# Performance work log

Measured on AMD Instinct MI355X. Metric: run time of the kernel, lower is better.

Reference implementation:

```python
import jax, jax.numpy as jnp
import numpy as np

B, T, C = 2, 4096, 1024
H = 16
D = C // H  # head_dim = 64


def setup_inputs() -> dict:
    key = jax.random.key(0)
    k1, k2, k3 = jax.random.split(key, 3)
    x = jax.random.normal(k1, (B, T, C), dtype=jnp.float32)
    W_qkv = jax.random.normal(k2, (3 * C, C), dtype=jnp.float32) * (1.0 / np.sqrt(C))
    W_out = jax.random.normal(k3, (C, C), dtype=jnp.float32) * (1.0 / np.sqrt(C))
    return {"x": x, "W_qkv": W_qkv, "W_out": W_out}


def reference(x, W_qkv, W_out):
    b, t, c = x.shape
    # qkv projection: torch Linear y = x @ W.T  -> (B,T,3C)
    qkv = jnp.einsum('btc,fc->btf', x, W_qkv)
    qkv = qkv.reshape(b, t, 3, H, D)
    q, k, v = qkv[:, :, 0], qkv[:, :, 1], qkv[:, :, 2]  # (B,T,H,D)
    q = q.transpose(0, 2, 1, 3)  # (B,H,T,D)
    k = k.transpose(0, 2, 1, 3)
    v = v.transpose(0, 2, 1, 3)
    scale = 1.0 / np.sqrt(D).astype(np.float32)
    att = jnp.einsum('bhqd,bhkd->bhqk', q, k) * scale  # (B,H,T,T)
    causal = jnp.tril(jnp.ones((t, t), dtype=bool))
    att = jnp.where(causal[None, None], att, jnp.float32(-jnp.inf))
    att = jax.nn.softmax(att, axis=-1)
    # dropout p=0.0 -> identity
    out = jnp.einsum('bhqk,bhkd->bhqd', att, v)  # (B,H,T,D)
    out = out.transpose(0, 2, 1, 3).reshape(b, t, c)
    return jnp.einsum('btc,oc->bto', out, W_out)
```

## Files before the change

kernel.cpp:

```cpp
#include <hip/hip_runtime.h>

constexpr int Bn = 2;
constexpr int Tn = 4096;
constexpr int Cn = 1024;
constexpr int Hn = 16;
constexpr int Dn = 64;

typedef __bf16 bf16x8 __attribute__((ext_vector_type(8)));
typedef float f32x4 __attribute__((ext_vector_type(4)));
typedef unsigned short u16x8 __attribute__((ext_vector_type(8)));

__device__ __forceinline__ unsigned short f2bf(float f) {
  unsigned int u = __float_as_uint(f);
  u += 0x7FFF + ((u >> 16) & 1);
  return (unsigned short)(u >> 16);
}

__device__ __forceinline__ unsigned short f2bf_hw(float f) {
  return __builtin_bit_cast(unsigned short, (__bf16)f);
}

__device__ __forceinline__ bf16x8 ld_bf8(const unsigned short* p) {
  return __builtin_bit_cast(bf16x8, *(const u16x8*)p);
}

__global__ void cvt_kernel(const float* __restrict__ in, unsigned short* __restrict__ out, int n4) {
  int i = blockIdx.x * blockDim.x + threadIdx.x;
  if (i >= n4) return;
  float4 v = ((const float4*)in)[i];
  ushort4 o;
  o.x = f2bf(v.x); o.y = f2bf(v.y); o.z = f2bf(v.z); o.w = f2bf(v.w);
  ((ushort4*)out)[i] = o;
}

template<int OUT_BF16>
__global__ __launch_bounds__(256) void gemm_bt(const unsigned short* __restrict__ A,
                                               const unsigned short* __restrict__ Bm,
                                               void* __restrict__ Cout,
                                               int M, int N, int K) {
  __shared__ __align__(16) unsigned short As[128][64];
  __shared__ __align__(16) unsigned short Bs[128][64];
  const int tid  = threadIdx.x;
  const int wave = tid >> 6;
  const int lane = tid & 63;
  const int wr   = (wave >> 1) * 64;
  const int wc   = (wave & 1) * 64;
  const int lrow = lane & 15;
  const int lk8  = (lane >> 4) << 3;

  const int nbx  = gridDim.x;
  const int nwg  = nbx * gridDim.y;
  const int orig = blockIdx.y * nbx + blockIdx.x;
  const int cid  = (orig & 7) * (nwg >> 3) + (orig >> 3);
  const int row0 = (cid / nbx) * 128;
  const int col0 = (cid % nbx) * 128;

  f32x4 acc[4][4];
  #pragma unroll
  for (int i = 0; i < 4; ++i)
    #pragma unroll
    for (int j = 0; j < 4; ++j)
      acc[i][j] = (f32x4){0.f, 0.f, 0.f, 0.f};

  for (int k0 = 0; k0 < K; k0 += 64) {
    const unsigned short* Ag = A  + (size_t)row0 * K + k0;
    const unsigned short* Bg = Bm + (size_t)col0 * K + k0;
    #pragma unroll
    for (int i = 0; i < 4; ++i) {
      int flat = (i * 256 + tid) * 8;
      int r = flat >> 6, c = flat & 63;
      __builtin_amdgcn_global_load_lds((const __attribute__((address_space(1))) void*)(Ag + (size_t)r * K + c),
                                       (__attribute__((address_space(3))) void*)(&As[r][c]), 16, 0, 0);
    }
    #pragma unroll
    for (int i = 0; i < 4; ++i) {
      int flat = (i * 256 + tid) * 8;
      int r = flat >> 6, c = flat & 63;
      __builtin_amdgcn_global_load_lds((const __attribute__((address_space(1))) void*)(Bg + (size_t)r * K + c),
                                       (__attribute__((address_space(3))) void*)(&Bs[r][c]), 16, 0, 0);
    }
    __syncthreads();

    #pragma unroll
    for (int ks = 0; ks < 2; ++ks) {
      bf16x8 af[4], bfr[4];
      #pragma unroll
      for (int i = 0; i < 4; ++i) af[i]  = ld_bf8(&As[wr + i * 16 + lrow][ks * 32 + lk8]);
      #pragma unroll
      for (int j = 0; j < 4; ++j) bfr[j] = ld_bf8(&Bs[wc + j * 16 + lrow][ks * 32 + lk8]);
      #pragma unroll
      for (int i = 0; i < 4; ++i)
        #pragma unroll
        for (int j = 0; j < 4; ++j)
          acc[i][j] = __builtin_amdgcn_mfma_f32_16x16x32_bf16(af[i], bfr[j], acc[i][j], 0, 0, 0);
    }
    __syncthreads();
  }

  const int rg = (lane >> 4) * 4;
  const int cl = lane & 15;
  #pragma unroll
  for (int i = 0; i < 4; ++i)
    #pragma unroll
    for (int j = 0; j < 4; ++j)
      #pragma unroll
      for (int rr = 0; rr < 4; ++rr) {
        int gm = row0 + wr + i * 16 + rg + rr;
        int gn = col0 + wc + j * 16 + cl;
        float v = acc[i][j][rr];
        if (OUT_BF16) ((unsigned short*)Cout)[(size_t)gm * N + gn] = f2bf(v);
        else          ((float*)Cout)[(size_t)gm * N + gn] = v;
      }
}

__global__ __launch_bounds__(256) void vtrans_kernel(const unsigned short* __restrict__ qkv,
                                                     unsigned short* __restrict__ vT) {
  __shared__ __align__(16) unsigned short L[64 * 64];
  const int tid = threadIdx.x;
  const int t0  = blockIdx.x * 64;
  const int bh  = blockIdx.y;
  const int b   = bh >> 4;
  const int h   = bh & 15;
  const unsigned short* src = qkv + (size_t)b * Tn * (3 * Cn) + 2 * Cn + h * Dn;

  #pragma unroll
  for (int i = 0; i < 2; ++i) {
    int flat = i * 256 + tid;
    int t = flat >> 3, c = flat & 7;
    int cs = c ^ ((t >> 3) & 7);
    __builtin_amdgcn_global_load_lds(
        (const __attribute__((address_space(1))) void*)(src + (size_t)(t0 + t) * (3 * Cn) + cs * 8),
        (__attribute__((address_space(3))) void*)(&L[flat * 8]), 16, 0, 0);
  }
  __syncthreads();

  #pragma unroll
  for (int i = 0; i < 2; ++i) {
    int flat = i * 256 + tid;
    int d = flat >> 3, tc = flat & 7;
    u16x8 o;
    #pragma unroll
    for (int j = 0; j < 8; ++j) {
      int t = tc * 8 + j;
      o[j] = L[t * 64 + (((d >> 3) ^ ((t >> 3) & 7)) << 3) + (d & 7)];
    }
    *(u16x8*)(vT + ((size_t)bh * 64 + d) * Tn + t0 + tc * 8) = o;
  }
}

__global__ __launch_bounds__(256) void attn_kernel(const unsigned short* __restrict__ qkv,
                                                   const unsigned short* __restrict__ vT,
                                                   unsigned short* __restrict__ outb) {
  __shared__ __align__(16) unsigned short Ks[2][4096];
  __shared__ __align__(16) unsigned short Vs[2][4096];
  __shared__ __align__(16) unsigned short Ps[4][1024];

  const int tid  = threadIdx.x;
  const int wave = tid >> 6;
  const int lane = tid & 63;
  const int cl   = lane & 15;
  const int g    = lane >> 4;
  const int lk8  = g << 3;
  const int rg   = g * 4;

  const int orig = blockIdx.y * gridDim.x + blockIdx.x;
  const int cid  = (orig & 7) * 256 + (orig >> 3);
  const int qt   = (63 - (cid & 63)) * 64;
  const int bh   = cid >> 6;
  const int b    = bh >> 4;
  const int h    = bh & 15;

  const unsigned short* qb  = qkv + (size_t)b * Tn * (3 * Cn) + h * Dn;
  const unsigned short* kb  = qb + Cn;
  const unsigned short* vtb = vT + (size_t)bh * Dn * Tn;

  bf16x8 qf[2];
  {
    const unsigned short* qr = qb + (size_t)(qt + wave * 16 + cl) * (3 * Cn) + lk8;
    qf[0] = ld_bf8(qr);
    qf[1] = ld_bf8(qr + 32);
    #pragma unroll
    for (int j = 0; j < 8; ++j) {
      qf[0][j] = qf[0][j] * (__bf16)0.125f;
      qf[1][j] = qf[1][j] * (__bf16)0.125f;
    }
  }

  f32x4 oacc[4];
  #pragma unroll
  for (int n = 0; n < 4; ++n) oacc[n] = (f32x4){0.f, 0.f, 0.f, 0.f};
  float mrun[4] = {-1e30f, -1e30f, -1e30f, -1e30f};
  float lrun[4] = {0.f, 0.f, 0.f, 0.f};

  #pragma unroll
  for (int i = 0; i < 2; ++i) {
    const int flat = i * 256 + tid;
    const int r    = flat >> 3;
    const int cg   = flat & 7;
    const int sw   = cg ^ (r & 7);
    __builtin_amdgcn_global_load_lds(
        (const __attribute__((address_space(1))) void*)(kb + (size_t)r * (3 * Cn) + sw * 8),
        (__attribute__((address_space(3))) void*)(&Ks[0][flat * 8]), 16, 0, 0);
    __builtin_amdgcn_global_load_lds(
        (const __attribute__((address_space(1))) void*)(vtb + (size_t)r * Tn + sw * 8),
        (__attribute__((address_space(3))) void*)(&Vs[0][flat * 8]), 16, 0, 0);
  }
  __syncthreads();

  const int nkv = qt / 64 + 1;
  for (int kt = 0; kt < nkv; ++kt) {
    const int kv0 = kt * 64;
    const int cur = kt & 1;
    const int nb  = cur ^ 1;
    const bool pre = (kt + 1 < nkv);

    if (pre) {
      const int kv1 = kv0 + 64;
      #pragma unroll
      for (int i = 0; i < 2; ++i) {
        const int flat = i * 256 + tid;
        const int r    = flat >> 3;
        const int cg   = flat & 7;
        const int sw   = cg ^ (r & 7);
        __builtin_amdgcn_global_load_lds(
            (const __attribute__((address_space(1))) void*)(kb + (size_t)(kv1 + r) * (3 * Cn) + sw * 8),
            (__attribute__((address_space(3))) void*)(&Ks[nb][flat * 8]), 16, 0, 0);
        __builtin_amdgcn_global_load_lds(
            (const __attribute__((address_space(1))) void*)(vtb + (size_t)r * Tn + kv1 + sw * 8),
            (__attribute__((address_space(3))) void*)(&Vs[nb][flat * 8]), 16, 0, 0);
      }
    }

    f32x4 s[4];
    #pragma unroll
    for (int n = 0; n < 4; ++n) s[n] = (f32x4){0.f, 0.f, 0.f, 0.f};
    __builtin_amdgcn_s_setprio(1);
    #pragma unroll
    for (int n = 0; n < 4; ++n)
      #pragma unroll
      for (int ks = 0; ks < 2; ++ks) {
        bf16x8 kf = ld_bf8(&Ks[cur][(n * 16 + cl) * 64 + (((ks * 4 + g) ^ (cl & 7)) << 3)]);
        s[n] = __builtin_amdgcn_mfma_f32_16x16x32_bf16(qf[ks], kf, s[n], 0, 0, 0);
      }
    __builtin_amdgcn_s_setprio(0);

    const bool diag = (kv0 == qt);
    if (diag) {
      #pragma unroll
      for (int n = 0; n < 4; ++n)
        #pragma unroll
        for (int rr = 0; rr < 4; ++rr) {
          int ql = wave * 16 + rg + rr;
          int kl = n * 16 + cl;
          if (kl > ql) s[n][rr] = -1e30f;
        }
    }

    float pmax[4];
    #pragma unroll
    for (int rr = 0; rr < 4; ++rr) {
      float mx = fmaxf(fmaxf(s[0][rr], s[1][rr]), fmaxf(s[2][rr], s[3][rr]));
      mx = fmaxf(mx, __shfl_xor(mx, 1));
      mx = fmaxf(mx, __shfl_xor(mx, 2));
      mx = fmaxf(mx, __shfl_xor(mx, 4));
      mx = fmaxf(mx, __shfl_xor(mx, 8));
      pmax[rr] = mx;
    }
    const bool need = (pmax[0] > mrun[0]) || (pmax[1] > mrun[1]) ||
                      (pmax[2] > mrun[2]) || (pmax[3] > mrun[3]);
    if (__any(need)) {
      #pragma unroll
      for (int rr = 0; rr < 4; ++rr) {
        float mnew  = fmaxf(mrun[rr], pmax[rr]);
        float alpha = __expf(mrun[rr] - mnew);
        mrun[rr] = mnew;
        float psum = 0.f;
        #pragma unroll
        for (int n = 0; n < 4; ++n) {
          float p = __expf(s[n][rr] - mnew);
          s[n][rr] = p;
          psum += p;
        }
        lrun[rr] = lrun[rr] * alpha + psum;
        #pragma unroll
        for (int n = 0; n < 4; ++n) oacc[n][rr] *= alpha;
      }
    } else {
      #pragma unroll
      for (int rr = 0; rr < 4; ++rr) {
        float psum = 0.f;
        #pragma unroll
        for (int n = 0; n < 4; ++n) {
          float p = __expf(s[n][rr] - mrun[rr]);
          s[n][rr] = p;
          psum += p;
        }
        lrun[rr] += psum;
      }
    }

    #pragma unroll
    for (int n = 0; n < 4; ++n)
      #pragma unroll
      for (int rr = 0; rr < 4; ++rr) {
        const int row  = rg + rr;
        const int slot = n * 2 + (cl >> 3);
        Ps[wave][row * 64 + ((slot ^ (row & 7)) << 3) + (cl & 7)] = f2bf_hw(s[n][rr]);
      }

    #pragma unroll
    for (int ks = 0; ks < 2; ++ks) {
      bf16x8 pa = ld_bf8(&Ps[wave][cl * 64 + (((ks * 4 + g) ^ (cl & 7)) << 3)]);
      __builtin_amdgcn_s_setprio(1);
      #pragma unroll
      for (int n = 0; n < 4; ++n) {
        bf16x8 vf = ld_bf8(&Vs[cur][(n * 16 + cl) * 64 + (((ks * 4 + g) ^ (cl & 7)) << 3)]);
        oacc[n] = __builtin_amdgcn_mfma_f32_16x16x32_bf16(pa, vf, oacc[n], 0, 0, 0);
      }
      __builtin_amdgcn_s_setprio(0);
    }

    __syncthreads();
  }

  #pragma unroll
  for (int rr = 0; rr < 4; ++rr) {
    lrun[rr] += __shfl_xor(lrun[rr], 1);
    lrun[rr] += __shfl_xor(lrun[rr], 2);
    lrun[rr] += __shfl_xor(lrun[rr], 4);
    lrun[rr] += __shfl_xor(lrun[rr], 8);
  }
  #pragma unroll
  for (int rr = 0; rr < 4; ++rr) {
    float inv = 1.0f / lrun[rr];
    int t = qt + wave * 16 + rg + rr;
    size_t rowo = ((size_t)b * Tn + t) * Cn + h * Dn;
    #pragma unroll
    for (int n = 0; n < 4; ++n)
      outb[rowo + n * 16 + cl] = f2bf_hw(oacc[n][rr] * inv);
  }
}

extern "C" void kernel_launch(void* const* d_in, const int* in_sizes, int n_in,
                              void* d_out, int out_size, void* d_ws, size_t ws_size,
                              hipStream_t stream) {
  const float* x    = (const float*)d_in[0];
  const float* Wqkv = (const float*)d_in[1];
  const float* Wout = (const float*)d_in[2];
  float* y = (float*)d_out;

  unsigned short* xb    = (unsigned short*)d_ws;
  unsigned short* wqkvb = xb    + (size_t)Bn * Tn * Cn;
  unsigned short* woutb = wqkvb + (size_t)3 * Cn * Cn;
  unsigned short* qkvb  = woutb + (size_t)Cn * Cn;
  unsigned short* attno = qkvb  + (size_t)Bn * Tn * 3 * Cn;

  const int M = Bn * Tn;

  {
    int n4 = (Bn * Tn * Cn) / 4;
    cvt_kernel<<<(n4 + 255) / 256, 256, 0, stream>>>(x, xb, n4);
  }
  {
    int n4 = (3 * Cn * Cn) / 4;
    cvt_kernel<<<(n4 + 255) / 256, 256, 0, stream>>>(Wqkv, wqkvb, n4);
  }
  {
    int n4 = (Cn * Cn) / 4;
    cvt_kernel<<<(n4 + 255) / 256, 256, 0, stream>>>(Wout, woutb, n4);
  }

  gemm_bt<1><<<dim3(3 * Cn / 128, M / 128), 256, 0, stream>>>(xb, wqkvb, qkvb, M, 3 * Cn, Cn);

  unsigned short* vT = xb;
  vtrans_kernel<<<dim3(Tn / 64, Bn * Hn), 256, 0, stream>>>(qkvb, vT);

  attn_kernel<<<dim3(Tn / 64, Bn * Hn), 256, 0, stream>>>(qkvb, vT, attno);

  gemm_bt<0><<<dim3(Cn / 128, M / 128), 256, 0, stream>>>(attno, woutb, y, M, Cn, Cn);

  (void)in_sizes; (void)n_in; (void)out_size; (void)ws_size;
}
```

Before: 413.0 us.

## Fuse V transpose into QKV GEMM epilogue and double attention query tile

The QKV GEMM epilogue now writes V directly in transposed per-head layout and pre-scales Q by softmax scale times log2(e), so the separate transpose kernel is dropped and attention can use exp2f. The attention kernel processes 128 query rows per block (32 per wave, two MFMA row groups) so each loaded K/V tile is reused twice. This cuts kernel launches and K/V traffic, at the cost of more registers, larger P shared buffer, fewer blocks and coarser causal work granularity.

```diff
diff --git a/kernel.cpp b/kernel.cpp
--- a/kernel.cpp
+++ b/kernel.cpp
@@ -33,10 +33,11 @@
   ((ushort4*)out)[i] = o;
 }
 
-template<int OUT_BF16>
+template<int MODE>
 __global__ __launch_bounds__(256) void gemm_bt(const unsigned short* __restrict__ A,
                                                const unsigned short* __restrict__ Bm,
                                                void* __restrict__ Cout,
+                                               unsigned short* __restrict__ vT,
                                                int M, int N, int K) {
   __shared__ __align__(16) unsigned short As[128][64];
   __shared__ __align__(16) unsigned short Bs[128][64];
@@ -99,52 +100,45 @@
 
   const int rg = (lane >> 4) * 4;
   const int cl = lane & 15;
-  #pragma unroll
-  for (int i = 0; i < 4; ++i)
-    #pragma unroll
-    for (int j = 0; j < 4; ++j)
-      #pragma unroll
-      for (int rr = 0; rr < 4; ++rr) {
-        int gm = row0 + wr + i * 16 + rg + rr;
-        int gn = col0 + wc + j * 16 + cl;
-        float v = acc[i][j][rr];
-        if (OUT_BF16) ((unsigned short*)Cout)[(size_t)gm * N + gn] = f2bf(v);
-        else          ((float*)Cout)[(size_t)gm * N + gn] = v;
-      }
-}
-
-__global__ __launch_bounds__(256) void vtrans_kernel(const unsigned short* __restrict__ qkv,
-                                                     unsigned short* __restrict__ vT) {
-  __shared__ __align__(16) unsigned short L[64 * 64];
-  const int tid = threadIdx.x;
-  const int t0  = blockIdx.x * 64;
-  const int bh  = blockIdx.y;
-  const int b   = bh >> 4;
-  const int h   = bh & 15;
-  const unsigned short* src = qkv + (size_t)b * Tn * (3 * Cn) + 2 * Cn + h * Dn;
-
-  #pragma unroll
-  for (int i = 0; i < 2; ++i) {
-    int flat = i * 256 + tid;
-    int t = flat >> 3, c = flat & 7;
-    int cs = c ^ ((t >> 3) & 7);
-    __builtin_amdgcn_global_load_lds(
-        (const __attribute__((address_space(1))) void*)(src + (size_t)(t0 + t) * (3 * Cn) + cs * 8),
-        (__attribute__((address_space(3))) void*)(&L[flat * 8]), 16, 0, 0);
-  }
-  __syncthreads();
-
-  #pragma unroll
-  for (int i = 0; i < 2; ++i) {
-    int flat = i * 256 + tid;
-    int d = flat >> 3, tc = flat & 7;
-    u16x8 o;
-    #pragma unroll
-    for (int j = 0; j < 8; ++j) {
-      int t = tc * 8 + j;
-      o[j] = L[t * 64 + (((d >> 3) ^ ((t >> 3) & 7)) << 3) + (d & 7)];
-    }
-    *(u16x8*)(vT + ((size_t)bh * 64 + d) * Tn + t0 + tc * 8) = o;
+  if constexpr (MODE == 2) {
+    if (col0 >= 2048) {
+      #pragma unroll
+      for (int i = 0; i < 4; ++i)
+        #pragma unroll
+        for (int j = 0; j < 4; ++j) {
+          int gm = row0 + wr + i * 16 + rg;
+          int gn = col0 - 2048 + wc + j * 16 + cl;
+          int hh = gn >> 6, dd = gn & 63;
+          int bb = gm >> 12, tt = gm & 4095;
+          ushort4 pk;
+          pk.x = f2bf(acc[i][j][0]); pk.y = f2bf(acc[i][j][1]);
+          pk.z = f2bf(acc[i][j][2]); pk.w = f2bf(acc[i][j][3]);
+          *(ushort4*)(vT + (((size_t)bb * 16 + hh) * 64 + dd) * (size_t)Tn + tt) = pk;
+        }
+    } else {
+      const float qs = (col0 < 1024) ? 0.18033688011112042f : 1.0f;
+      #pragma unroll
+      for (int i = 0; i < 4; ++i)
+        #pragma unroll
+        for (int j = 0; j < 4; ++j)
+          #pragma unroll
+          for (int rr = 0; rr < 4; ++rr) {
+            int gm = row0 + wr + i * 16 + rg + rr;
+            int gn = col0 + wc + j * 16 + cl;
+            ((unsigned short*)Cout)[(size_t)gm * N + gn] = f2bf(acc[i][j][rr] * qs);
+          }
+    }
+  } else {
+    #pragma unroll
+    for (int i = 0; i < 4; ++i)
+      #pragma unroll
+      for (int j = 0; j < 4; ++j)
+        #pragma unroll
+        for (int rr = 0; rr < 4; ++rr) {
+          int gm = row0 + wr + i * 16 + rg + rr;
+          int gn = col0 + wc + j * 16 + cl;
+          ((float*)Cout)[(size_t)gm * N + gn] = acc[i][j][rr];
+        }
   }
 }
 
@@ -153,7 +147,7 @@
                                                    unsigned short* __restrict__ outb) {
   __shared__ __align__(16) unsigned short Ks[2][4096];
   __shared__ __align__(16) unsigned short Vs[2][4096];
-  __shared__ __align__(16) unsigned short Ps[4][1024];
+  __shared__ __align__(16) unsigned short Ps[4][2048];
 
   const int tid  = threadIdx.x;
   const int wave = tid >> 6;
@@ -164,9 +158,9 @@
   const int rg   = g * 4;
 
   const int orig = blockIdx.y * gridDim.x + blockIdx.x;
-  const int cid  = (orig & 7) * 256 + (orig >> 3);
-  const int qt   = (63 - (cid & 63)) * 64;
-  const int bh   = cid >> 6;
+  const int cid  = (orig & 7) * 128 + (orig >> 3);
+  const int qt   = (31 - (cid & 31)) * 128;
+  const int bh   = cid >> 5;
   const int b    = bh >> 4;
   const int h    = bh & 15;
 
@@ -174,23 +168,26 @@
   const unsigned short* kb  = qb + Cn;
   const unsigned short* vtb = vT + (size_t)bh * Dn * Tn;
 
-  bf16x8 qf[2];
+  bf16x8 qf[2][2];
   {
-    const unsigned short* qr = qb + (size_t)(qt + wave * 16 + cl) * (3 * Cn) + lk8;
-    qf[0] = ld_bf8(qr);
-    qf[1] = ld_bf8(qr + 32);
-    #pragma unroll
-    for (int j = 0; j < 8; ++j) {
-      qf[0][j] = qf[0][j] * (__bf16)0.125f;
-      qf[1][j] = qf[1][j] * (__bf16)0.125f;
-    }
-  }
-
-  f32x4 oacc[4];
-  #pragma unroll
-  for (int n = 0; n < 4; ++n) oacc[n] = (f32x4){0.f, 0.f, 0.f, 0.f};
-  float mrun[4] = {-1e30f, -1e30f, -1e30f, -1e30f};
-  float lrun[4] = {0.f, 0.f, 0.f, 0.f};
+    const unsigned short* qr0 = qb + (size_t)(qt + wave * 32 + cl) * (3 * Cn) + lk8;
+    qf[0][0] = ld_bf8(qr0);
+    qf[0][1] = ld_bf8(qr0 + 32);
+    const unsigned short* qr1 = qr0 + (size_t)16 * (3 * Cn);
+    qf[1][0] = ld_bf8(qr1);
+    qf[1][1] = ld_bf8(qr1 + 32);
+  }
+
+  f32x4 oacc[2][4];
+  #pragma unroll
+  for (int u = 0; u < 2; ++u)
+    #pragma unroll
+    for (int n = 0; n < 4; ++n) oacc[u][n] = (f32x4){0.f, 0.f, 0.f, 0.f};
+  float mrun[2][4], lrun[2][4];
+  #pragma unroll
+  for (int u = 0; u < 2; ++u)
+    #pragma unroll
+    for (int rr = 0; rr < 4; ++rr) { mrun[u][rr] = -1e30f; lrun[u][rr] = 0.f; }
 
   #pragma unroll
   for (int i = 0; i < 2; ++i) {
@@ -207,7 +204,7 @@
   }
   __syncthreads();
 
-  const int nkv = qt / 64 + 1;
+  const int nkv = qt / 64 + 2;
   for (int kt = 0; kt < nkv; ++kt) {
     const int kv0 = kt * 64;
     const int cur = kt & 1;
@@ -231,91 +228,108 @@
       }
     }
 
-    f32x4 s[4];
-    #pragma unroll
-    for (int n = 0; n < 4; ++n) s[n] = (f32x4){0.f, 0.f, 0.f, 0.f};
+    f32x4 s[2][4];
+    #pragma unroll
+    for (int u = 0; u < 2; ++u)
+      #pragma unroll
+      for (int n = 0; n < 4; ++n) s[u][n] = (f32x4){0.f, 0.f, 0.f, 0.f};
     __builtin_amdgcn_s_setprio(1);
     #pragma unroll
     for (int n = 0; n < 4; ++n)
       #pragma unroll
       for (int ks = 0; ks < 2; ++ks) {
         bf16x8 kf = ld_bf8(&Ks[cur][(n * 16 + cl) * 64 + (((ks * 4 + g) ^ (cl & 7)) << 3)]);
-        s[n] = __builtin_amdgcn_mfma_f32_16x16x32_bf16(qf[ks], kf, s[n], 0, 0, 0);
+        s[0][n] = __builtin_amdgcn_mfma_f32_16x16x32_bf16(qf[0][ks], kf, s[0][n], 0, 0, 0);
+        s[1][n] = __builtin_amdgcn_mfma_f32_16x16x32_bf16(qf[1][ks], kf, s[1][n], 0, 0, 0);
       }
     __builtin_amdgcn_s_setprio(0);
 
-    const bool diag = (kv0 == qt);
-    if (diag) {
+    if (kv0 >= qt) {
+      #pragma unroll
+      for (int u = 0; u < 2; ++u)
+        #pragma unroll
+        for (int n = 0; n < 4; ++n)
+          #pragma unroll
+          for (int rr = 0; rr < 4; ++rr) {
+            int qg = qt + wave * 32 + u * 16 + rg + rr;
+            int kg = kv0 + n * 16 + cl;
+            if (kg > qg) s[u][n][rr] = -1e30f;
+          }
+    }
+
+    float pmax[2][4];
+    #pragma unroll
+    for (int u = 0; u < 2; ++u)
+      #pragma unroll
+      for (int rr = 0; rr < 4; ++rr) {
+        float mx = fmaxf(fmaxf(s[u][0][rr], s[u][1][rr]), fmaxf(s[u][2][rr], s[u][3][rr]));
+        mx = fmaxf(mx, __shfl_xor(mx, 1));
+        mx = fmaxf(mx, __shfl_xor(mx, 2));
+        mx = fmaxf(mx, __shfl_xor(mx, 4));
+        mx = fmaxf(mx, __shfl_xor(mx, 8));
+        pmax[u][rr] = mx;
+      }
+    bool need = false;
+    #pragma unroll
+    for (int u = 0; u < 2; ++u)
+      #pragma unroll
+      for (int rr = 0; rr < 4; ++rr) need = need || (pmax[u][rr] > mrun[u][rr]);
+    if (__any(need)) {
+      #pragma unroll
+      for (int u = 0; u < 2; ++u)
+        #pragma unroll
+        for (int rr = 0; rr < 4; ++rr) {
+          float mnew  = fmaxf(mrun[u][rr], pmax[u][rr]);
+          float alpha = exp2f(mrun[u][rr] - mnew);
+          mrun[u][rr] = mnew;
+          float psum = 0.f;
+          #pragma unroll
+          for (int n = 0; n < 4; ++n) {
+            float p = exp2f(s[u][n][rr] - mnew);
+            s[u][n][rr] = p;
+            psum += p;
+          }
+          lrun[u][rr] = lrun[u][rr] * alpha + psum;
+          #pragma unroll
+          for (int n = 0; n < 4; ++n) oacc[u][n][rr] *= alpha;
+        }
+    } else {
+      #pragma unroll
+      for (int u = 0; u < 2; ++u)
+        #pragma unroll
+        for (int rr = 0; rr < 4; ++rr) {
+          float psum = 0.f;
+          #pragma unroll
+          for (int n = 0; n < 4; ++n) {
+            float p = exp2f(s[u][n][rr] - mrun[u][rr]);
+            s[u][n][rr] = p;
+            psum += p;
+          }
+          lrun[u][rr] += psum;
+        }
+    }
+
+    #pragma unroll
+    for (int u = 0; u < 2; ++u)
       #pragma unroll
       for (int n = 0; n < 4; ++n)
         #pragma unroll
         for (int rr = 0; rr < 4; ++rr) {
-          int ql = wave * 16 + rg + rr;
-          int kl = n * 16 + cl;
-          if (kl > ql) s[n][rr] = -1e30f;
-        }
-    }
-
-    float pmax[4];
-    #pragma unroll
-    for (int rr = 0; rr < 4; ++rr) {
-      float mx = fmaxf(fmaxf(s[0][rr], s[1][rr]), fmaxf(s[2][rr], s[3][rr]));
-      mx = fmaxf(mx, __shfl_xor(mx, 1));
-      mx = fmaxf(mx, __shfl_xor(mx, 2));
-      mx = fmaxf(mx, __shfl_xor(mx, 4));
-      mx = fmaxf(mx, __shfl_xor(mx, 8));
-      pmax[rr] = mx;
-    }
-    const bool need = (pmax[0] > mrun[0]) || (pmax[1] > mrun[1]) ||
-                      (pmax[2] > mrun[2]) || (pmax[3] > mrun[3]);
-    if (__any(need)) {
-      #pragma unroll
-      for (int rr = 0; rr < 4; ++rr) {
-        float mnew  = fmaxf(mrun[rr], pmax[rr]);
-        float alpha = __expf(mrun[rr] - mnew);
-        mrun[rr] = mnew;
-        float psum = 0.f;
-        #pragma unroll
-        for (int n = 0; n < 4; ++n) {
-          float p = __expf(s[n][rr] - mnew);
-          s[n][rr] = p;
-          psum += p;
-        }
-        lrun[rr] = lrun[rr] * alpha + psum;
-        #pragma unroll
-        for (int n = 0; n < 4; ++n) oacc[n][rr] *= alpha;
-      }
-    } else {
-      #pragma unroll
-      for (int rr = 0; rr < 4; ++rr) {
-        float psum = 0.f;
-        #pragma unroll
-        for (int n = 0; n < 4; ++n) {
-          float p = __expf(s[n][rr] - mrun[rr]);
-          s[n][rr] = p;
-          psum += p;
-        }
-        lrun[rr] += psum;
-      }
-    }
-
-    #pragma unroll
-    for (int n = 0; n < 4; ++n)
-      #pragma unroll
-      for (int rr = 0; rr < 4; ++rr) {
-        const int row  = rg + rr;
-        const int slot = n * 2 + (cl >> 3);
-        Ps[wave][row * 64 + ((slot ^ (row & 7)) << 3) + (cl & 7)] = f2bf_hw(s[n][rr]);
-      }
+          const int row  = u * 16 + rg + rr;
+          const int slot = n * 2 + (cl >> 3);
+          Ps[wave][row * 64 + ((slot ^ (row & 7)) << 3) + (cl & 7)] = f2bf_hw(s[u][n][rr]);
+        }
 
     #pragma unroll
     for (int ks = 0; ks < 2; ++ks) {
-      bf16x8 pa = ld_bf8(&Ps[wave][cl * 64 + (((ks * 4 + g) ^ (cl & 7)) << 3)]);
+      bf16x8 pa0 = ld_bf8(&Ps[wave][cl * 64 + (((ks * 4 + g) ^ (cl & 7)) << 3)]);
+      bf16x8 pa1 = ld_bf8(&Ps[wave][(16 + cl) * 64 + (((ks * 4 + g) ^ (cl & 7)) << 3)]);
       __builtin_amdgcn_s_setprio(1);
       #pragma unroll
       for (int n = 0; n < 4; ++n) {
         bf16x8 vf = ld_bf8(&Vs[cur][(n * 16 + cl) * 64 + (((ks * 4 + g) ^ (cl & 7)) << 3)]);
-        oacc[n] = __builtin_amdgcn_mfma_f32_16x16x32_bf16(pa, vf, oacc[n], 0, 0, 0);
+        oacc[0][n] = __builtin_amdgcn_mfma_f32_16x16x32_bf16(pa0, vf, oacc[0][n], 0, 0, 0);
+        oacc[1][n] = __builtin_amdgcn_mfma_f32_16x16x32_bf16(pa1, vf, oacc[1][n], 0, 0, 0);
       }
       __builtin_amdgcn_s_setprio(0);
     }
@@ -324,21 +338,25 @@
   }
 
   #pragma unroll
-  for (int rr = 0; rr < 4; ++rr) {
-    lrun[rr] += __shfl_xor(lrun[rr], 1);
-    lrun[rr] += __shfl_xor(lrun[rr], 2);
-    lrun[rr] += __shfl_xor(lrun[rr], 4);
-    lrun[rr] += __shfl_xor(lrun[rr], 8);
-  }
-  #pragma unroll
-  for (int rr = 0; rr < 4; ++rr) {
-    float inv = 1.0f / lrun[rr];
-    int t = qt + wave * 16 + rg + rr;
-    size_t rowo = ((size_t)b * Tn + t) * Cn + h * Dn;
-    #pragma unroll
-    for (int n = 0; n < 4; ++n)
-      outb[rowo + n * 16 + cl] = f2bf_hw(oacc[n][rr] * inv);
-  }
+  for (int u = 0; u < 2; ++u)
+    #pragma unroll
+    for (int rr = 0; rr < 4; ++rr) {
+      lrun[u][rr] += __shfl_xor(lrun[u][rr], 1);
+      lrun[u][rr] += __shfl_xor(lrun[u][rr], 2);
+      lrun[u][rr] += __shfl_xor(lrun[u][rr], 4);
+      lrun[u][rr] += __shfl_xor(lrun[u][rr], 8);
+    }
+  #pragma unroll
+  for (int u = 0; u < 2; ++u)
+    #pragma unroll
+    for (int rr = 0; rr < 4; ++rr) {
+      float inv = 1.0f / lrun[u][rr];
+      int t = qt + wave * 32 + u * 16 + rg + rr;
+      size_t rowo = ((size_t)b * Tn + t) * Cn + h * Dn;
+      #pragma unroll
+      for (int n = 0; n < 4; ++n)
+        outb[rowo + n * 16 + cl] = f2bf_hw(oacc[u][n][rr] * inv);
+    }
 }
 
 extern "C" void kernel_launch(void* const* d_in, const int* in_sizes, int n_in,
@@ -353,7 +371,7 @@
   unsigned short* wqkvb = xb    + (size_t)Bn * Tn * Cn;
   unsigned short* woutb = wqkvb + (size_t)3 * Cn * Cn;
   unsigned short* qkvb  = woutb + (size_t)Cn * Cn;
-  unsigned short* attno = qkvb  + (size_t)Bn * Tn * 3 * Cn;
+  unsigned short* vtb   = qkvb  + (size_t)Bn * Tn * 3 * Cn;
 
   const int M = Bn * Tn;
 
@@ -370,14 +388,11 @@
     cvt_kernel<<<(n4 + 255) / 256, 256, 0, stream>>>(Wout, woutb, n4);
   }
 
-  gemm_bt<1><<<dim3(3 * Cn / 128, M / 128), 256, 0, stream>>>(xb, wqkvb, qkvb, M, 3 * Cn, Cn);
-
-  unsigned short* vT = xb;
-  vtrans_kernel<<<dim3(Tn / 64, Bn * Hn), 256, 0, stream>>>(qkvb, vT);
-
-  attn_kernel<<<dim3(Tn / 64, Bn * Hn), 256, 0, stream>>>(qkvb, vT, attno);
-
-  gemm_bt<0><<<dim3(Cn / 128, M / 128), 256, 0, stream>>>(attno, woutb, y, M, Cn, Cn);
+  gemm_bt<2><<<dim3(3 * Cn / 128, M / 128), 256, 0, stream>>>(xb, wqkvb, qkvb, vtb, M, 3 * Cn, Cn);
+
+  attn_kernel<<<dim3(Tn / 128, Bn * Hn), 256, 0, stream>>>(qkvb, vtb, xb);
+
+  gemm_bt<0><<<dim3(Cn / 128, M / 128), 256, 0, stream>>>(xb, woutb, y, nullptr, M, Cn, Cn);
 
   (void)in_sizes; (void)n_in; (void)out_size; (void)ws_size;
 }
```

Measured after the change: 578.4 us. 1.4x slower.

## Fuse V transpose and Q scaling into QKV GEMM epilogue, use exp2 softmax

Applied to the files above, without the earlier changes.

The QKV GEMM epilogue now writes the V columns straight into a transposed per-head layout, which removes the separate vtrans kernel and its extra read and write of V. It also multiplies Q by scale*log2(e) before rounding to bf16, so the attention kernel no longer scales Q and can call exp2f instead of __expf. The transposed V stores are 4-element packed writes with a large stride and may coalesce worse. Folding the scale in before rounding changes bf16 rounding slightly.

```diff
diff --git a/kernel.cpp b/kernel.cpp
--- a/kernel.cpp
+++ b/kernel.cpp
@@ -33,10 +33,11 @@
   ((ushort4*)out)[i] = o;
 }
 
-template<int OUT_BF16>
+template<int MODE>
 __global__ __launch_bounds__(256) void gemm_bt(const unsigned short* __restrict__ A,
                                                const unsigned short* __restrict__ Bm,
                                                void* __restrict__ Cout,
+                                               unsigned short* __restrict__ vT,
                                                int M, int N, int K) {
   __shared__ __align__(16) unsigned short As[128][64];
   __shared__ __align__(16) unsigned short Bs[128][64];
@@ -99,52 +100,45 @@
 
   const int rg = (lane >> 4) * 4;
   const int cl = lane & 15;
-  #pragma unroll
-  for (int i = 0; i < 4; ++i)
-    #pragma unroll
-    for (int j = 0; j < 4; ++j)
-      #pragma unroll
-      for (int rr = 0; rr < 4; ++rr) {
-        int gm = row0 + wr + i * 16 + rg + rr;
-        int gn = col0 + wc + j * 16 + cl;
-        float v = acc[i][j][rr];
-        if (OUT_BF16) ((unsigned short*)Cout)[(size_t)gm * N + gn] = f2bf(v);
-        else          ((float*)Cout)[(size_t)gm * N + gn] = v;
-      }
-}
-
-__global__ __launch_bounds__(256) void vtrans_kernel(const unsigned short* __restrict__ qkv,
-                                                     unsigned short* __restrict__ vT) {
-  __shared__ __align__(16) unsigned short L[64 * 64];
-  const int tid = threadIdx.x;
-  const int t0  = blockIdx.x * 64;
-  const int bh  = blockIdx.y;
-  const int b   = bh >> 4;
-  const int h   = bh & 15;
-  const unsigned short* src = qkv + (size_t)b * Tn * (3 * Cn) + 2 * Cn + h * Dn;
-
-  #pragma unroll
-  for (int i = 0; i < 2; ++i) {
-    int flat = i * 256 + tid;
-    int t = flat >> 3, c = flat & 7;
-    int cs = c ^ ((t >> 3) & 7);
-    __builtin_amdgcn_global_load_lds(
-        (const __attribute__((address_space(1))) void*)(src + (size_t)(t0 + t) * (3 * Cn) + cs * 8),
-        (__attribute__((address_space(3))) void*)(&L[flat * 8]), 16, 0, 0);
-  }
-  __syncthreads();
-
-  #pragma unroll
-  for (int i = 0; i < 2; ++i) {
-    int flat = i * 256 + tid;
-    int d = flat >> 3, tc = flat & 7;
-    u16x8 o;
-    #pragma unroll
-    for (int j = 0; j < 8; ++j) {
-      int t = tc * 8 + j;
-      o[j] = L[t * 64 + (((d >> 3) ^ ((t >> 3) & 7)) << 3) + (d & 7)];
-    }
-    *(u16x8*)(vT + ((size_t)bh * 64 + d) * Tn + t0 + tc * 8) = o;
+  if constexpr (MODE == 2) {
+    if (col0 >= 2048) {
+      #pragma unroll
+      for (int i = 0; i < 4; ++i)
+        #pragma unroll
+        for (int j = 0; j < 4; ++j) {
+          int gm = row0 + wr + i * 16 + rg;
+          int gn = col0 - 2048 + wc + j * 16 + cl;
+          int hh = gn >> 6, dd = gn & 63;
+          int bb = gm >> 12, tt = gm & 4095;
+          ushort4 pk;
+          pk.x = f2bf(acc[i][j][0]); pk.y = f2bf(acc[i][j][1]);
+          pk.z = f2bf(acc[i][j][2]); pk.w = f2bf(acc[i][j][3]);
+          *(ushort4*)(vT + (((size_t)bb * 16 + hh) * 64 + dd) * (size_t)Tn + tt) = pk;
+        }
+    } else {
+      const float qs = (col0 < 1024) ? 0.18033688011112042f : 1.0f;
+      #pragma unroll
+      for (int i = 0; i < 4; ++i)
+        #pragma unroll
+        for (int j = 0; j < 4; ++j)
+          #pragma unroll
+          for (int rr = 0; rr < 4; ++rr) {
+            int gm = row0 + wr + i * 16 + rg + rr;
+            int gn = col0 + wc + j * 16 + cl;
+            ((unsigned short*)Cout)[(size_t)gm * N + gn] = f2bf(acc[i][j][rr] * qs);
+          }
+    }
+  } else {
+    #pragma unroll
+    for (int i = 0; i < 4; ++i)
+      #pragma unroll
+      for (int j = 0; j < 4; ++j)
+        #pragma unroll
+        for (int rr = 0; rr < 4; ++rr) {
+          int gm = row0 + wr + i * 16 + rg + rr;
+          int gn = col0 + wc + j * 16 + cl;
+          ((float*)Cout)[(size_t)gm * N + gn] = acc[i][j][rr];
+        }
   }
 }
 
@@ -179,11 +173,6 @@
     const unsigned short* qr = qb + (size_t)(qt + wave * 16 + cl) * (3 * Cn) + lk8;
     qf[0] = ld_bf8(qr);
     qf[1] = ld_bf8(qr + 32);
-    #pragma unroll
-    for (int j = 0; j < 8; ++j) {
-      qf[0][j] = qf[0][j] * (__bf16)0.125f;
-      qf[1][j] = qf[1][j] * (__bf16)0.125f;
-    }
   }
 
   f32x4 oacc[4];
@@ -272,12 +261,12 @@
       #pragma unroll
       for (int rr = 0; rr < 4; ++rr) {
         float mnew  = fmaxf(mrun[rr], pmax[rr]);
-        float alpha = __expf(mrun[rr] - mnew);
+        float alpha = exp2f(mrun[rr] - mnew);
         mrun[rr] = mnew;
         float psum = 0.f;
         #pragma unroll
         for (int n = 0; n < 4; ++n) {
-          float p = __expf(s[n][rr] - mnew);
+          float p = exp2f(s[n][rr] - mnew);
           s[n][rr] = p;
           psum += p;
         }
@@ -291,7 +280,7 @@
         float psum = 0.f;
         #pragma unroll
         for (int n = 0; n < 4; ++n) {
-          float p = __expf(s[n][rr] - mrun[rr]);
+          float p = exp2f(s[n][rr] - mrun[rr]);
           s[n][rr] = p;
           psum += p;
         }
@@ -353,7 +342,7 @@
   unsigned short* wqkvb = xb    + (size_t)Bn * Tn * Cn;
   unsigned short* woutb = wqkvb + (size_t)3 * Cn * Cn;
   unsigned short* qkvb  = woutb + (size_t)Cn * Cn;
-  unsigned short* attno = qkvb  + (size_t)Bn * Tn * 3 * Cn;
+  unsigned short* vtb   = qkvb  + (size_t)Bn * Tn * 3 * Cn;
 
   const int M = Bn * Tn;
 
@@ -370,14 +359,11 @@
     cvt_kernel<<<(n4 + 255) / 256, 256, 0, stream>>>(Wout, woutb, n4);
   }
 
-  gemm_bt<1><<<dim3(3 * Cn / 128, M / 128), 256, 0, stream>>>(xb, wqkvb, qkvb, M, 3 * Cn, Cn);
-
-  unsigned short* vT = xb;
-  vtrans_kernel<<<dim3(Tn / 64, Bn * Hn), 256, 0, stream>>>(qkvb, vT);
-
-  attn_kernel<<<dim3(Tn / 64, Bn * Hn), 256, 0, stream>>>(qkvb, vT, attno);
-
-  gemm_bt<0><<<dim3(Cn / 128, M / 128), 256, 0, stream>>>(attno, woutb, y, M, Cn, Cn);
+  gemm_bt<2><<<dim3(3 * Cn / 128, M / 128), 256, 0, stream>>>(xb, wqkvb, qkvb, vtb, M, 3 * Cn, Cn);
+
+  attn_kernel<<<dim3(Tn / 64, Bn * Hn), 256, 0, stream>>>(qkvb, vtb, xb);
+
+  gemm_bt<0><<<dim3(Cn / 128, M / 128), 256, 0, stream>>>(xb, woutb, y, nullptr, M, Cn, Cn);
 
   (void)in_sizes; (void)n_in; (void)out_size; (void)ws_size;
 }
```

After: 431.1 us. 1.04x slower.
